# Performance work log

Measured on AMD Instinct MI355X. Metric: run time of the kernel, lower is better.

## Reference

```python
import jax, jax.numpy as jnp
import numpy as np

B, S, C_IN, C_OUT = 8, 2048, 512, 512

def setup_inputs() -> dict:
    key = jax.random.key(0)
    k1, k2, k3, k4 = jax.random.split(key, 4)
    sc = 1.0 / np.sqrt(C_IN)
    return {
        "x": jax.random.normal(k1, (B, S, C_IN), dtype=jnp.float32),
        "Wq": jax.random.normal(k2, (C_OUT, C_IN), dtype=jnp.float32) * sc,
        "Wk": jax.random.normal(k3, (C_OUT, C_IN), dtype=jnp.float32) * sc,
        "Wv": jax.random.normal(k4, (C_OUT, C_IN), dtype=jnp.float32) * sc,
    }

def reference(x, Wq, Wk, Wv):
    # x: [B,S,Cin]; weights [Cout,Cin] (torch Linear convention, no bias)
    C = Wq.shape[0]
    dk = jnp.sqrt(jnp.float32(1.0) / C)  # torch: sqrt(1/out_features)
    q = jnp.einsum('bsi,oi->bso', x, Wq)
    k = jnp.einsum('bsi,oi->bso', x, Wk)
    v = jnp.einsum('bsi,oi->bso', x, Wv)
    phi_q = jax.nn.elu(q * dk) + 1.0
    phi_k = jax.nn.elu(k * dk) + 1.0
    b = x.shape[0]
    mem0 = jnp.zeros((b, C, C), x.dtype)   # running sum of phi_k v^T
    zeta0 = jnp.zeros((b, C), x.dtype)     # running sum of phi_k
    def step(carry, inp):
        mem, zeta = carry
        pq, pk, vv = inp                    # each [B,C]
        dm = pk[:, :, None] * vv[:, None, :]              # [B,C,C]
        scale = jnp.einsum('bc,bc->b', pq, pk + zeta) + 1e-5
        num = jnp.einsum('bc,bcd->bd', pq, dm + mem)
        y = num / scale[:, None]
        # state updates are under torch.no_grad -> detach
        new_mem = jax.lax.stop_gradient(mem + dm)
        new_zeta = jax.lax.stop_gradient(zeta + pk)
        return (new_mem, new_zeta), y
    xs = (phi_q.transpose(1, 0, 2), phi_k.transpose(1, 0, 2), v.transpose(1, 0, 2))
    _, ys = jax.lax.scan(step, (mem0, zeta0), xs)  # ys: [S,B,C]
    return ys.transpose(1, 0, 2)                   # [B,S,C]
```

## Files before the change

kernel.cpp:

```cpp
#include <hip/hip_runtime.h>


constexpr int Bn  = 8;
constexpr int Sn  = 2048;
constexpr int Cn  = 512;
constexpr int Tn  = 128;
constexpr int NCn = 16;
constexpr float DKf = 0.04419417382415922f;

typedef __attribute__((ext_vector_type(8))) short bf16x8;
typedef __attribute__((ext_vector_type(4))) float f32x4;

__device__ __forceinline__ unsigned short f2bf(float f) {
  unsigned u = __float_as_uint(f);
  u = (u + 0x7fffu + ((u >> 16) & 1u)) >> 16;
  return (unsigned short)u;
}
__device__ __forceinline__ float bf2f(unsigned short h) {
  return __uint_as_float(((unsigned)h) << 16);
}
__device__ __forceinline__ float phi_f(float u) {
  float s = u * DKf;
  return s > 0.0f ? s + 1.0f : __expf(s);
}

__global__ __launch_bounds__(256) void k_cast(
    const float* __restrict__ x, const float* __restrict__ Wq,
    const float* __restrict__ Wk, const float* __restrict__ Wv,
    unsigned short* __restrict__ xb, unsigned short* __restrict__ Wb)
{
  const int bid = blockIdx.x;
  const float* src;
  unsigned short* dst;
  size_t i8;
  if (bid < 4096) {
    i8 = ((size_t)bid * 256 + threadIdx.x) * 8;
    src = x; dst = xb;
  } else {
    const size_t f = ((size_t)(bid - 4096) * 256 + threadIdx.x) * 8;
    const int z = (int)(f >> 18);
    src = (z == 0) ? Wq : (z == 1 ? Wk : Wv);
    dst = Wb + ((size_t)z << 18);
    i8 = f & ((1u << 18) - 1);
  }
  float4 a = *(const float4*)&src[i8];
  float4 b = *(const float4*)&src[i8 + 4];
  uint4 o;
  o.x = (unsigned)f2bf(a.x) | ((unsigned)f2bf(a.y) << 16);
  o.y = (unsigned)f2bf(a.z) | ((unsigned)f2bf(a.w) << 16);
  o.z = (unsigned)f2bf(b.x) | ((unsigned)f2bf(b.y) << 16);
  o.w = (unsigned)f2bf(b.z) | ((unsigned)f2bf(b.w) << 16);
  *(uint4*)&dst[i8] = o;
}

__device__ __forceinline__ void stageA256(const unsigned short* __restrict__ g,
                                          unsigned short* lds, int wid, int lane) {
#pragma unroll
  for (int cc = 0; cc < 2; ++cc) {
    const int row = cc * 128 + wid * 16 + (lane >> 2);
    const int ks  = (lane & 3) ^ ((row >> 1) & 3);
    __builtin_amdgcn_global_load_lds(
        (const __attribute__((address_space(1))) void*)(g + (size_t)row * Cn + ks * 8),
        (__attribute__((address_space(3))) void*)(lds + (cc * 128 + wid * 16) * 32),
        16, 0, 0);
  }
}
__device__ __forceinline__ void stageB128w8(const unsigned short* __restrict__ g,
                                            unsigned short* lds, int wid, int lane) {
  const int row = wid * 16 + (lane >> 2);
  const int ks  = (lane & 3) ^ ((row >> 1) & 3);
  __builtin_amdgcn_global_load_lds(
      (const __attribute__((address_space(1))) void*)(g + (size_t)row * Cn + ks * 8),
      (__attribute__((address_space(3))) void*)(lds + (wid * 16) * 32), 16, 0, 0);
}

__global__ __launch_bounds__(512) void k_proj(
    const unsigned short* __restrict__ xb, const unsigned short* __restrict__ Wb,
    unsigned short* __restrict__ PQ, unsigned short* __restrict__ PK,
    unsigned short* __restrict__ PKt, unsigned short* __restrict__ Vt,
    float* __restrict__ zsum)
{
  __shared__ unsigned short Al[3 * 8192], Bl[3 * 4096];
  __shared__ float zbuf[4][128];
  const int bid = blockIdx.x;
  const int xcd = bid & 7, idx = bid >> 3;
  const int n = idx & 3, z = (idx >> 2) % 3, mloc = idx / 12;
  const int n0 = n * 128, m0 = (xcd * 8 + mloc) * 256;
  const int t = threadIdx.x, wid = t >> 6, lane = t & 63;
  const int wm = wid >> 1, wn = wid & 1;
  const int fr = lane & 15, kb = lane >> 4;
  f32x4 acc[4][4];
  const f32x4 zero = {0.f, 0.f, 0.f, 0.f};
#pragma unroll
  for (int m = 0; m < 4; ++m)
#pragma unroll
    for (int nn = 0; nn < 4; ++nn) acc[m][nn] = zero;

  const unsigned short* Ag = xb + (size_t)m0 * Cn;
  const unsigned short* Bg = Wb + (size_t)z * Cn * Cn + (size_t)n0 * Cn;

  stageA256(Ag, Al, wid, lane);
  stageB128w8(Bg, Bl, wid, lane);
  stageA256(Ag + 32, Al + 8192, wid, lane);
  stageB128w8(Bg + 32, Bl + 4096, wid, lane);
  int cur = 0;
  for (int kt = 0; kt < 16; ++kt) {
    if (kt + 2 < 16) {
      const int nx2 = (cur + 2 >= 3) ? cur - 1 : cur + 2;
      stageA256(Ag + (kt + 2) * 32, Al + nx2 * 8192, wid, lane);
      stageB128w8(Bg + (kt + 2) * 32, Bl + nx2 * 4096, wid, lane);
      asm volatile("s_waitcnt vmcnt(6)" ::: "memory");
    } else if (kt + 1 < 16) {
      asm volatile("s_waitcnt vmcnt(3)" ::: "memory");
    } else {
      asm volatile("s_waitcnt vmcnt(0)" ::: "memory");
    }
    __builtin_amdgcn_s_barrier();
    asm volatile("" ::: "memory");
    const unsigned short* Ac = Al + cur * 8192;
    const unsigned short* Bc = Bl + cur * 4096;
    bf16x8 af[4], bf[4];
#pragma unroll
    for (int m = 0; m < 4; ++m) {
      const int r = wm * 64 + m * 16 + fr;
      af[m] = *(const bf16x8*)&Ac[r * 32 + ((kb ^ ((r >> 1) & 3)) << 3)];
    }
#pragma unroll
    for (int nn = 0; nn < 4; ++nn) {
      const int r = wn * 64 + nn * 16 + fr;
      bf[nn] = *(const bf16x8*)&Bc[r * 32 + ((kb ^ ((r >> 1) & 3)) << 3)];
    }
    __builtin_amdgcn_s_setprio(1);
#pragma unroll
    for (int m = 0; m < 4; ++m)
#pragma unroll
      for (int nn = 0; nn < 4; ++nn)
        acc[m][nn] = __builtin_amdgcn_mfma_f32_16x16x32_bf16(af[m], bf[nn], acc[m][nn], 0, 0, 0);
    __builtin_amdgcn_s_setprio(0);
    __builtin_amdgcn_s_barrier();
    asm volatile("" ::: "memory");
    cur = (cur + 1 >= 3) ? 0 : cur + 1;
  }

  float ps[4] = {0.f, 0.f, 0.f, 0.f};
#pragma unroll
  for (int m = 0; m < 4; ++m)
#pragma unroll
    for (int nn = 0; nn < 4; ++nn) {
      const int row0 = m0 + wm * 64 + m * 16 + ((lane >> 4) << 2);
      const int col  = n0 + wn * 64 + nn * 16 + fr;
      f32x4 v = acc[m][nn];
      if (z == 0) {
#pragma unroll
        for (int j = 0; j < 4; ++j)
          PQ[(size_t)(row0 + j) * Cn + col] = f2bf(phi_f(v[j]));
      } else if (z == 1) {
        ushort4 p;
#pragma unroll
        for (int j = 0; j < 4; ++j) {
          unsigned short u = f2bf(phi_f(v[j]));
          PK[(size_t)(row0 + j) * Cn + col] = u;
          (&p.x)[j] = u;
          ps[nn] += bf2f(u);
        }
        const int b = row0 >> 11, tq = row0 & (Sn - 1);
        *(ushort4*)&PKt[((size_t)b * Cn + col) * Sn + tq] = p;
      } else {
        ushort4 p;
#pragma unroll
        for (int j = 0; j < 4; ++j) (&p.x)[j] = f2bf(v[j]);
        const int b = row0 >> 11, tq = row0 & (Sn - 1);
        *(ushort4*)&Vt[((size_t)b * Cn + col) * Sn + tq] = p;
      }
    }

  if (z == 1) {
#pragma unroll
    for (int nn = 0; nn < 4; ++nn) {
      float v = ps[nn];
      v += __shfl_xor(v, 16); v += __shfl_xor(v, 32);
      if (lane < 16) zbuf[wm][wn * 64 + nn * 16 + lane] = v;
    }
    __syncthreads();
    if (t < 256) {
      const int c = t >> 7, colI = t & 127;
      const int b = m0 >> 11, ch = ((m0 >> 7) & 15) + c;
      zsum[((size_t)b * NCn + ch) * Cn + n0 + colI] =
          zbuf[2 * c][colI] + zbuf[2 * c + 1][colI];
    }
  }
}

__device__ __forceinline__ void stageA64(const unsigned short* __restrict__ g,
                                         unsigned short* lds, int wid, int lane) {
  const int row = wid * 16 + (lane >> 2);
  const int ks  = (lane & 3) ^ ((row >> 1) & 3);
  __builtin_amdgcn_global_load_lds(
      (const __attribute__((address_space(1))) void*)(g + (size_t)row * Cn + ks * 8),
      (__attribute__((address_space(3))) void*)(lds + wid * 512), 16, 0, 0);
}
__device__ __forceinline__ void stageB128(const unsigned short* __restrict__ g,
                                          unsigned short* lds, int wid, int lane) {
#pragma unroll
  for (int e = 0; e < 2; ++e) {
    const int row = e * 64 + wid * 16 + (lane >> 2);
    const int ks  = (lane & 3) ^ ((row >> 1) & 3);
    __builtin_amdgcn_global_load_lds(
        (const __attribute__((address_space(1))) void*)(g + (size_t)row * Cn + ks * 8),
        (__attribute__((address_space(3))) void*)(lds + e * 2048 + wid * 512),
        16, 0, 0);
  }
}

__device__ __forceinline__ void stage64x128(const unsigned short* __restrict__ g,
                                            int ld, unsigned short* lds,
                                            int wid, int lane) {
#pragma unroll
  for (int i = 0; i < 4; ++i) {
    const int row = wid * 16 + i * 4 + (lane >> 4);
    const int s   = (lane & 15) ^ (row & 7);
    const unsigned short* src = g + (size_t)row * ld + s * 8;
    unsigned short* dst = lds + (size_t)(wid * 16 + i * 4) * 128;
    __builtin_amdgcn_global_load_lds(
        (const __attribute__((address_space(1))) void*)src,
        (__attribute__((address_space(3))) void*)dst, 16, 0, 0);
  }
}

__global__ __launch_bounds__(256) void k_gk(
    const unsigned short* __restrict__ PQ, const unsigned short* __restrict__ PK,
    const float* __restrict__ zsum,
    unsigned short* __restrict__ Abuf, float* __restrict__ scale,
    const unsigned short* __restrict__ PKt, const unsigned short* __restrict__ Vt,
    unsigned short* __restrict__ Mpre)
{
  __shared__ unsigned short smem[32768];
  const int t = threadIdx.x, wid = t >> 6, lane = t & 63;
  const int fr = lane & 15, kb = lane >> 4;
  const f32x4 zero = {0.f, 0.f, 0.f, 0.f};

  if (blockIdx.x < 512) {
    unsigned short* Al = smem;
    unsigned short* Bl = smem + 16384;
    const int bid = blockIdx.x;
    const int b = bid & 7, idx = bid >> 3;
    const int d0 = (idx & 7) * 64, c0 = (idx >> 3) * 64;
    const int wm = wid >> 1, wn = wid & 1;
    f32x4 acc[2][2];
#pragma unroll
    for (int m = 0; m < 2; ++m)
#pragma unroll
      for (int n = 0; n < 2; ++n) acc[m][n] = zero;
    const unsigned short* Ag = PKt + ((size_t)b * Cn + c0) * Sn;
    const unsigned short* Bg = Vt  + ((size_t)b * Cn + d0) * Sn;
    stage64x128(Ag, Sn, Al, wid, lane);
    stage64x128(Bg, Sn, Bl, wid, lane);
    int cur = 0;
    for (int ch = 0; ch < NCn; ++ch) {
      const int nxt = cur ^ 1;
      if (ch + 1 < NCn) {
        stage64x128(Ag + (ch + 1) * Tn, Sn, Al + nxt * 8192, wid, lane);
        stage64x128(Bg + (ch + 1) * Tn, Sn, Bl + nxt * 8192, wid, lane);
        asm volatile("s_waitcnt vmcnt(8)" ::: "memory");
      } else {
        asm volatile("s_waitcnt vmcnt(0)" ::: "memory");
      }
      __builtin_amdgcn_s_barrier();
      asm volatile("" ::: "memory");
      if (ch > 0) {
#pragma unroll
        for (int m = 0; m < 2; ++m)
#pragma unroll
          for (int n = 0; n < 2; ++n) {
            const int c_row = c0 + wm * 32 + m * 16 + (kb << 2);
            const int d     = d0 + wn * 32 + n * 16 + fr;
            ushort4 p;
#pragma unroll
            for (int j = 0; j < 4; ++j) (&p.x)[j] = f2bf(acc[m][n][j]);
            *(ushort4*)&Mpre[((size_t)(b * NCn + ch) * Cn + d) * Cn + c_row] = p;
          }
      }
      const unsigned short* Ac = Al + cur * 8192;
      const unsigned short* Bc = Bl + cur * 8192;
      __builtin_amdgcn_s_setprio(1);
#pragma unroll
      for (int kt = 0; kt < 4; ++kt) {
        bf16x8 af[2], bf[2];
#pragma unroll
        for (int m = 0; m < 2; ++m) {
          const int r = wm * 32 + m * 16 + fr;
          af[m] = *(const bf16x8*)&Ac[r * 128 + (((kt * 4 + kb) ^ (r & 7)) << 3)];
        }
#pragma unroll
        for (int n = 0; n < 2; ++n) {
          const int r = wn * 32 + n * 16 + fr;
          bf[n] = *(const bf16x8*)&Bc[r * 128 + (((kt * 4 + kb) ^ (r & 7)) << 3)];
        }
#pragma unroll
        for (int m = 0; m < 2; ++m)
#pragma unroll
          for (int n = 0; n < 2; ++n)
            acc[m][n] = __builtin_amdgcn_mfma_f32_16x16x32_bf16(af[m], bf[n], acc[m][n], 0, 0, 0);
      }
      __builtin_amdgcn_s_setprio(0);
      __builtin_amdgcn_s_barrier();
      asm volatile("" ::: "memory");
      cur = nxt;
    }
  } else {
    unsigned short* Asl = smem;
    unsigned short* Bsl = smem + 6144;
    float* rsmem = (float*)(smem + 18432);
    float* zpl   = rsmem + 256;
    const int g = blockIdx.x - 512;
    const int i0 = (g & 1) * 64, ch = (g >> 1) & 15, b = g >> 5;
    const unsigned short* Aq = PQ + ((size_t)(b * Sn + ch * Tn + i0)) * Cn;
    const unsigned short* Bk = PK + ((size_t)(b * Sn + ch * Tn)) * Cn;
    f32x4 acc[4][2];
#pragma unroll
    for (int m = 0; m < 4; ++m)
#pragma unroll
      for (int n = 0; n < 2; ++n) acc[m][n] = zero;

    stageA64(Aq, Asl, wid, lane);
    stageB128(Bk, Bsl, wid, lane);
    stageA64(Aq + 32, Asl + 2048, wid, lane);
    stageB128(Bk + 32, Bsl + 4096, wid, lane);
    int cur = 0;
    for (int kt = 0; kt < 16; ++kt) {
      if (kt + 2 < 16) {
        const int nx2 = (cur + 2 >= 3) ? cur - 1 : cur + 2;
        stageA64(Aq + (kt + 2) * 32, Asl + nx2 * 2048, wid, lane);
        stageB128(Bk + (kt + 2) * 32, Bsl + nx2 * 4096, wid, lane);
        asm volatile("s_waitcnt vmcnt(6)" ::: "memory");
      } else if (kt + 1 < 16) {
        asm volatile("s_waitcnt vmcnt(3)" ::: "memory");
      } else {
        asm volatile("s_waitcnt vmcnt(0)" ::: "memory");
      }
      __builtin_amdgcn_s_barrier();
      asm volatile("" ::: "memory");
      const unsigned short* Ac = Asl + cur * 2048;
      const unsigned short* Bc = Bsl + cur * 4096;
      bf16x8 af[4], bf[2];
#pragma unroll
      for (int m = 0; m < 4; ++m) {
        const int r = m * 16 + fr;
        af[m] = *(const bf16x8*)&Ac[r * 32 + ((kb ^ ((r >> 1) & 3)) << 3)];
      }
#pragma unroll
      for (int n = 0; n < 2; ++n) {
        const int c = wid * 32 + n * 16 + fr;
        bf[n] = *(const bf16x8*)&Bc[c * 32 + ((kb ^ ((c >> 1) & 3)) << 3)];
      }
      __builtin_amdgcn_s_setprio(1);
#pragma unroll
      for (int m = 0; m < 4; ++m)
#pragma unroll
        for (int n = 0; n < 2; ++n)
          acc[m][n] = __builtin_amdgcn_mfma_f32_16x16x32_bf16(af[m], bf[n], acc[m][n], 0, 0, 0);
      __builtin_amdgcn_s_setprio(0);
      __builtin_amdgcn_s_barrier();
      asm volatile("" ::: "memory");
      cur = (cur + 1 >= 3) ? 0 : cur + 1;
    }

    float rsum[4][4];
#pragma unroll
    for (int m = 0; m < 4; ++m)
#pragma unroll
      for (int j = 0; j < 4; ++j) rsum[m][j] = 0.f;
#pragma unroll
    for (int m = 0; m < 4; ++m)
#pragma unroll
      for (int n = 0; n < 2; ++n) {
        f32x4 v = acc[m][n];
#pragma unroll
        for (int j = 0; j < 4; ++j) {
          const int row_g = i0 + m * 16 + kb * 4 + j;
          const int col   = wid * 32 + n * 16 + fr;
          unsigned short u = (col <= row_g) ? f2bf(v[j]) : 0;
          Abuf[((size_t)(b * NCn + ch) * Tn + row_g) * Tn + col] = u;
          rsum[m][j] += bf2f(u);
        }
      }
#pragma unroll
    for (int m = 0; m < 4; ++m)
#pragma unroll
      for (int j = 0; j < 4; ++j) {
        float r = rsum[m][j];
        r += __shfl_xor(r, 1); r += __shfl_xor(r, 2);
        r += __shfl_xor(r, 4); r += __shfl_xor(r, 8);
        if (fr == 0) rsmem[wid * 64 + m * 16 + kb * 4 + j] = r;
      }
#pragma unroll
    for (int e = 0; e < 2; ++e) {
      const int c = t + e * 256;
      float s = 0.f;
      for (int ch2 = 0; ch2 < ch; ++ch2)
        s += zsum[((size_t)b * NCn + ch2) * Cn + c];
      zpl[c] = s;
    }
    __syncthreads();
    const int row = t >> 2, q4 = (t & 3) * 128;
    const unsigned short* pq = Aq + (size_t)row * Cn + q4;
    float dacc = 0.f;
    for (int i = 0; i < 128; i += 8) {
      uint4 q = *(const uint4*)(pq + i);
      dacc += bf2f((unsigned short)(q.x & 0xffff)) * zpl[q4 + i + 0]
            + bf2f((unsigned short)(q.x >> 16))    * zpl[q4 + i + 1]
            + bf2f((unsigned short)(q.y & 0xffff)) * zpl[q4 + i + 2]
            + bf2f((unsigned short)(q.y >> 16))    * zpl[q4 + i + 3]
            + bf2f((unsigned short)(q.z & 0xffff)) * zpl[q4 + i + 4]
            + bf2f((unsigned short)(q.z >> 16))    * zpl[q4 + i + 5]
            + bf2f((unsigned short)(q.w & 0xffff)) * zpl[q4 + i + 6]
            + bf2f((unsigned short)(q.w >> 16))    * zpl[q4 + i + 7];
    }
    dacc += __shfl_xor(dacc, 1);
    dacc += __shfl_xor(dacc, 2);
    if ((t & 3) == 0)
      scale[(size_t)b * Sn + ch * Tn + i0 + row] =
          rsmem[0 * 64 + row] + rsmem[1 * 64 + row] +
          rsmem[2 * 64 + row] + rsmem[3 * 64 + row] + dacc + 1e-5f;
  }
}

__device__ __forceinline__ void stage128x32(const unsigned short* __restrict__ g,
                                            int ld, unsigned short* lds,
                                            int wid, int lane) {
#pragma unroll
  for (int cc = 0; cc < 2; ++cc) {
    const int row = cc * 64 + wid * 16 + (lane >> 2);
    const int ks  = (lane & 3) ^ ((row >> 1) & 3);
    const unsigned short* src = g + (size_t)row * ld + ks * 8;
    unsigned short* dst = lds + (size_t)(cc * 256 + wid * 64) * 8;
    __builtin_amdgcn_global_load_lds(
        (const __attribute__((address_space(1))) void*)src,
        (__attribute__((address_space(3))) void*)dst, 16, 0, 0);
  }
}

__global__ __launch_bounds__(256) void k_avinter(
    const unsigned short* __restrict__ Abuf, const unsigned short* __restrict__ Vt,
    const unsigned short* __restrict__ PQ, const unsigned short* __restrict__ Mpre,
    const float* __restrict__ scale, float* __restrict__ out)
{
  __shared__ unsigned short Al[3 * 128 * 32], Bl[3 * 128 * 32];
  const int bid = blockIdx.x;
  const int logical = (bid & 7) * 64 + (bid >> 3);
  const int d0 = (logical & 3) * 128;
  const int ch = (logical >> 2) & 15;
  const int b  = logical >> 6;
  const int t0 = ch * Tn;
  const int t = threadIdx.x, wid = t >> 6, lane = t & 63;
  const int wm = wid >> 1, wn = wid & 1;
  const int fr = lane & 15, kb = lane >> 4;
  f32x4 acc[4][4];
  const f32x4 zero = {0.f, 0.f, 0.f, 0.f};
#pragma unroll
  for (int m = 0; m < 4; ++m)
#pragma unroll
    for (int n = 0; n < 4; ++n) acc[m][n] = zero;

  const unsigned short* Aintra = Abuf + (size_t)(b * NCn + ch) * Tn * Tn;
  const unsigned short* Bintra = Vt + ((size_t)b * Cn + d0) * Sn + t0;
  const unsigned short* Ainter = PQ + ((size_t)b * Sn + t0) * Cn;
  const unsigned short* Binter = Mpre + ((size_t)(b * NCn + ch) * Cn + d0) * Cn;
  auto srcA = [&](int kt) { return (kt < 4) ? Aintra + kt * 32 : Ainter + (kt - 4) * 32; };
  auto srcB = [&](int kt) { return (kt < 4) ? Bintra + kt * 32 : Binter + (kt - 4) * 32; };
  auto ldA  = [&](int kt) { return (kt < 4) ? Tn : Cn; };
  auto ldB  = [&](int kt) { return (kt < 4) ? Sn : Cn; };
  const int nkt = (ch > 0) ? 20 : 4;

  stage128x32(srcA(0), ldA(0), Al, wid, lane);
  stage128x32(srcB(0), ldB(0), Bl, wid, lane);
  stage128x32(srcA(1), ldA(1), Al + 4096, wid, lane);
  stage128x32(srcB(1), ldB(1), Bl + 4096, wid, lane);
  int cur = 0;
  for (int kt = 0; kt < nkt; ++kt) {
    if (kt + 2 < nkt) {
      const int nx2 = (cur + 2 >= 3) ? cur - 1 : cur + 2;
      stage128x32(srcA(kt + 2), ldA(kt + 2), Al + nx2 * 4096, wid, lane);
      stage128x32(srcB(kt + 2), ldB(kt + 2), Bl + nx2 * 4096, wid, lane);
      asm volatile("s_waitcnt vmcnt(8)" ::: "memory");
    } else if (kt + 1 < nkt) {
      asm volatile("s_waitcnt vmcnt(4)" ::: "memory");
    } else {
      asm volatile("s_waitcnt vmcnt(0)" ::: "memory");
    }
    __builtin_amdgcn_s_barrier();
    asm volatile("" ::: "memory");
    const unsigned short* Ac = Al + cur * 4096;
    const unsigned short* Bc = Bl + cur * 4096;
    bf16x8 af[4], bf[4];
#pragma unroll
    for (int m = 0; m < 4; ++m) {
      const int r = wm * 64 + m * 16 + fr;
      af[m] = *(const bf16x8*)&Ac[r * 32 + ((kb ^ ((r >> 1) & 3)) << 3)];
    }
#pragma unroll
    for (int n = 0; n < 4; ++n) {
      const int r = wn * 64 + n * 16 + fr;
      bf[n] = *(const bf16x8*)&Bc[r * 32 + ((kb ^ ((r >> 1) & 3)) << 3)];
    }
    __builtin_amdgcn_s_setprio(1);
#pragma unroll
    for (int m = 0; m < 4; ++m)
#pragma unroll
      for (int n = 0; n < 4; ++n)
        acc[m][n] = __builtin_amdgcn_mfma_f32_16x16x32_bf16(af[m], bf[n], acc[m][n], 0, 0, 0);
    __builtin_amdgcn_s_setprio(0);
    __builtin_amdgcn_s_barrier();
    asm volatile("" ::: "memory");
    cur = (cur + 1 >= 3) ? 0 : cur + 1;
  }

#pragma unroll
  for (int m = 0; m < 4; ++m)
#pragma unroll
    for (int n = 0; n < 4; ++n) {
      const int row0 = t0 + wm * 64 + m * 16 + ((lane >> 4) << 2);
      const int col  = d0 + wn * 64 + n * 16 + (lane & 15);
      f32x4 v = acc[m][n];
#pragma unroll
      for (int j = 0; j < 4; ++j) {
        const size_t sidx = (size_t)b * Sn + row0 + j;
        out[sidx * Cn + col] = v[j] / scale[sidx];
      }
    }
}

extern "C" void kernel_launch(void* const* d_in, const int* in_sizes, int n_in,
                              void* d_out, int out_size, void* d_ws, size_t ws_size,
                              hipStream_t stream)
{
  const float* x  = (const float*)d_in[0];
  const float* Wq = (const float*)d_in[1];
  const float* Wk = (const float*)d_in[2];
  const float* Wv = (const float*)d_in[3];
  float* out = (float*)d_out;

  unsigned short* xb   = (unsigned short*)d_ws;
  unsigned short* Wb   = xb   + (size_t)Bn * Sn * Cn;
  unsigned short* PQ   = Wb   + (size_t)3 * Cn * Cn;
  unsigned short* PK   = PQ   + (size_t)Bn * Sn * Cn;
  unsigned short* PKt  = PK   + (size_t)Bn * Sn * Cn;
  unsigned short* Vt   = PKt  + (size_t)Bn * Sn * Cn;
  unsigned short* Abuf = Vt   + (size_t)Bn * Sn * Cn;
  unsigned short* Mpre = Abuf + (size_t)Bn * NCn * Tn * Tn;
  float* scale = (float*)(Mpre + (size_t)Bn * NCn * Cn * Cn);
  float* zsum  = scale + (size_t)Bn * Sn;
  (void)ws_size; (void)in_sizes; (void)n_in; (void)out_size;

  hipLaunchKernelGGL(k_cast, dim3(4096 + 384), dim3(256), 0, stream, x, Wq, Wk, Wv, xb, Wb);
  hipLaunchKernelGGL(k_proj, dim3(768), dim3(512), 0, stream, xb, Wb, PQ, PK, PKt, Vt, zsum);
  hipLaunchKernelGGL(k_gk, dim3(768), dim3(256), 0, stream,
                     PQ, PK, zsum, Abuf, scale, PKt, Vt, Mpre);
  hipLaunchKernelGGL(k_avinter, dim3(512), dim3(256), 0, stream, Abuf, Vt, PQ, Mpre, scale, out);
}
```

Baseline: 124.9 us.

## Retile projection GEMM to 128x128 blocks with 64-wide K double buffering

The projection kernel changes from 256x128 tiles with 8 waves and a triple-buffered K=32 pipeline to 128x128 tiles with 4 waves and a double-buffered K=64 pipeline. The LDS swizzle is rewritten for 64-element rows, and the grid doubles to 1536 blocks. The goal is more blocks per CU and fewer barrier steps per K iteration for better occupancy and latency hiding. The cost is less A/B reuse per block and only one tile of prefetch lookahead instead of two.

```diff
diff --git a/kernel.cpp b/kernel.cpp
--- a/kernel.cpp
+++ b/kernel.cpp
@@ -53,39 +53,33 @@
   *(uint4*)&dst[i8] = o;
 }
 
-__device__ __forceinline__ void stageA256(const unsigned short* __restrict__ g,
-                                          unsigned short* lds, int wid, int lane) {
-#pragma unroll
-  for (int cc = 0; cc < 2; ++cc) {
-    const int row = cc * 128 + wid * 16 + (lane >> 2);
-    const int ks  = (lane & 3) ^ ((row >> 1) & 3);
+__device__ __forceinline__ void stage128x64(const unsigned short* __restrict__ g,
+                                            int ld, unsigned short* lds,
+                                            int wid, int lane) {
+#pragma unroll
+  for (int e = 0; e < 4; ++e) {
+    const int row = e * 32 + wid * 8 + (lane >> 3);
+    const int ks  = (lane & 7) ^ (row & 7);
+    const unsigned short* src = g + (size_t)row * ld + ks * 8;
+    unsigned short* dst = lds + (size_t)(e * 256 + wid * 64) * 8;
     __builtin_amdgcn_global_load_lds(
-        (const __attribute__((address_space(1))) void*)(g + (size_t)row * Cn + ks * 8),
-        (__attribute__((address_space(3))) void*)(lds + (cc * 128 + wid * 16) * 32),
-        16, 0, 0);
-  }
-}
-__device__ __forceinline__ void stageB128w8(const unsigned short* __restrict__ g,
-                                            unsigned short* lds, int wid, int lane) {
-  const int row = wid * 16 + (lane >> 2);
-  const int ks  = (lane & 3) ^ ((row >> 1) & 3);
-  __builtin_amdgcn_global_load_lds(
-      (const __attribute__((address_space(1))) void*)(g + (size_t)row * Cn + ks * 8),
-      (__attribute__((address_space(3))) void*)(lds + (wid * 16) * 32), 16, 0, 0);
-}
-
-__global__ __launch_bounds__(512) void k_proj(
+        (const __attribute__((address_space(1))) void*)src,
+        (__attribute__((address_space(3))) void*)dst, 16, 0, 0);
+  }
+}
+
+__global__ __launch_bounds__(256) void k_proj(
     const unsigned short* __restrict__ xb, const unsigned short* __restrict__ Wb,
     unsigned short* __restrict__ PQ, unsigned short* __restrict__ PK,
     unsigned short* __restrict__ PKt, unsigned short* __restrict__ Vt,
     float* __restrict__ zsum)
 {
-  __shared__ unsigned short Al[3 * 8192], Bl[3 * 4096];
-  __shared__ float zbuf[4][128];
+  __shared__ unsigned short Al[2 * 8192], Bl[2 * 8192];
+  __shared__ float zbuf[2][128];
   const int bid = blockIdx.x;
   const int xcd = bid & 7, idx = bid >> 3;
   const int n = idx & 3, z = (idx >> 2) % 3, mloc = idx / 12;
-  const int n0 = n * 128, m0 = (xcd * 8 + mloc) * 256;
+  const int n0 = n * 128, m0 = (xcd * 16 + mloc) * 128;
   const int t = threadIdx.x, wid = t >> 6, lane = t & 63;
   const int wm = wid >> 1, wn = wid & 1;
   const int fr = lane & 15, kb = lane >> 4;
@@ -99,47 +93,46 @@
   const unsigned short* Ag = xb + (size_t)m0 * Cn;
   const unsigned short* Bg = Wb + (size_t)z * Cn * Cn + (size_t)n0 * Cn;
 
-  stageA256(Ag, Al, wid, lane);
-  stageB128w8(Bg, Bl, wid, lane);
-  stageA256(Ag + 32, Al + 8192, wid, lane);
-  stageB128w8(Bg + 32, Bl + 4096, wid, lane);
+  stage128x64(Ag, Cn, Al, wid, lane);
+  stage128x64(Bg, Cn, Bl, wid, lane);
   int cur = 0;
-  for (int kt = 0; kt < 16; ++kt) {
-    if (kt + 2 < 16) {
-      const int nx2 = (cur + 2 >= 3) ? cur - 1 : cur + 2;
-      stageA256(Ag + (kt + 2) * 32, Al + nx2 * 8192, wid, lane);
-      stageB128w8(Bg + (kt + 2) * 32, Bl + nx2 * 4096, wid, lane);
-      asm volatile("s_waitcnt vmcnt(6)" ::: "memory");
-    } else if (kt + 1 < 16) {
-      asm volatile("s_waitcnt vmcnt(3)" ::: "memory");
+  for (int kt = 0; kt < 8; ++kt) {
+    const int nxt = cur ^ 1;
+    if (kt + 1 < 8) {
+      stage128x64(Ag + (kt + 1) * 64, Cn, Al + nxt * 8192, wid, lane);
+      stage128x64(Bg + (kt + 1) * 64, Cn, Bl + nxt * 8192, wid, lane);
+      asm volatile("s_waitcnt vmcnt(8)" ::: "memory");
     } else {
       asm volatile("s_waitcnt vmcnt(0)" ::: "memory");
     }
     __builtin_amdgcn_s_barrier();
     asm volatile("" ::: "memory");
     const unsigned short* Ac = Al + cur * 8192;
-    const unsigned short* Bc = Bl + cur * 4096;
-    bf16x8 af[4], bf[4];
-#pragma unroll
-    for (int m = 0; m < 4; ++m) {
-      const int r = wm * 64 + m * 16 + fr;
-      af[m] = *(const bf16x8*)&Ac[r * 32 + ((kb ^ ((r >> 1) & 3)) << 3)];
-    }
-#pragma unroll
-    for (int nn = 0; nn < 4; ++nn) {
-      const int r = wn * 64 + nn * 16 + fr;
-      bf[nn] = *(const bf16x8*)&Bc[r * 32 + ((kb ^ ((r >> 1) & 3)) << 3)];
-    }
-    __builtin_amdgcn_s_setprio(1);
-#pragma unroll
-    for (int m = 0; m < 4; ++m)
-#pragma unroll
-      for (int nn = 0; nn < 4; ++nn)
-        acc[m][nn] = __builtin_amdgcn_mfma_f32_16x16x32_bf16(af[m], bf[nn], acc[m][nn], 0, 0, 0);
-    __builtin_amdgcn_s_setprio(0);
+    const unsigned short* Bc = Bl + cur * 8192;
+#pragma unroll
+    for (int kk = 0; kk < 2; ++kk) {
+      bf16x8 af[4], bf[4];
+#pragma unroll
+      for (int m = 0; m < 4; ++m) {
+        const int r = wm * 64 + m * 16 + fr;
+        af[m] = *(const bf16x8*)&Ac[r * 64 + (((kk * 4 + kb) ^ (r & 7)) << 3)];
+      }
+#pragma unroll
+      for (int nn = 0; nn < 4; ++nn) {
+        const int r = wn * 64 + nn * 16 + fr;
+        bf[nn] = *(const bf16x8*)&Bc[r * 64 + (((kk * 4 + kb) ^ (r & 7)) << 3)];
+      }
+      __builtin_amdgcn_s_setprio(1);
+#pragma unroll
+      for (int m = 0; m < 4; ++m)
+#pragma unroll
+        for (int nn = 0; nn < 4; ++nn)
+          acc[m][nn] = __builtin_amdgcn_mfma_f32_16x16x32_bf16(af[m], bf[nn], acc[m][nn], 0, 0, 0);
+      __builtin_amdgcn_s_setprio(0);
+    }
     __builtin_amdgcn_s_barrier();
     asm volatile("" ::: "memory");
-    cur = (cur + 1 >= 3) ? 0 : cur + 1;
+    cur = nxt;
   }
 
   float ps[4] = {0.f, 0.f, 0.f, 0.f};
@@ -182,11 +175,9 @@
       if (lane < 16) zbuf[wm][wn * 64 + nn * 16 + lane] = v;
     }
     __syncthreads();
-    if (t < 256) {
-      const int c = t >> 7, colI = t & 127;
-      const int b = m0 >> 11, ch = ((m0 >> 7) & 15) + c;
-      zsum[((size_t)b * NCn + ch) * Cn + n0 + colI] =
-          zbuf[2 * c][colI] + zbuf[2 * c + 1][colI];
+    if (t < 128) {
+      const int b = m0 >> 11, ch = (m0 >> 7) & 15;
+      zsum[((size_t)b * NCn + ch) * Cn + n0 + t] = zbuf[0][t] + zbuf[1][t];
     }
   }
 }
@@ -553,7 +544,7 @@
   (void)ws_size; (void)in_sizes; (void)n_in; (void)out_size;
 
   hipLaunchKernelGGL(k_cast, dim3(4096 + 384), dim3(256), 0, stream, x, Wq, Wk, Wv, xb, Wb);
-  hipLaunchKernelGGL(k_proj, dim3(768), dim3(512), 0, stream, xb, Wb, PQ, PK, PKt, Vt, zsum);
+  hipLaunchKernelGGL(k_proj, dim3(1536), dim3(256), 0, stream, xb, Wb, PQ, PK, PKt, Vt, zsum);
   hipLaunchKernelGGL(k_gk, dim3(768), dim3(256), 0, stream,
                      PQ, PK, zsum, Abuf, scale, PKt, Vt, Mpre);
   hipLaunchKernelGGL(k_avinter, dim3(512), dim3(256), 0, stream, Abuf, Vt, PQ, Mpre, scale, out);
```

Result: faster. 118.3 us, median of 2 (-5.3%).
